# Kernel tuning notes

Hardware: AMD Instinct MI355X
Metric: run time of the kernel (lower is better)

## Reference

```python
import jax, jax.numpy as jnp
import numpy as np
from jax import lax

B, L, DIN, DOUT, K = 8, 4096, 256, 256, 3


def _gates(x, W, b, k):
    # x: [B, L, Din] -> conv over time, channels-first like torch Conv1d
    xt = jnp.transpose(x, (0, 2, 1))  # [B, Din, L]
    pad = (k - 1) // 2
    g = lax.conv_general_dilated(xt, W, window_strides=(1,), padding=[(pad, pad)],
                                 dimension_numbers=("NCH", "OIH", "NCH"))
    g = g + b[None, :, None]
    g = jnp.transpose(g, (0, 2, 1))  # [B, L, 3*Dout]
    f, o, z = jnp.split(g, 3, axis=-1)
    return jax.nn.sigmoid(f), jax.nn.sigmoid(o), jnp.tanh(z)


def _fo_pool(f, z, init_cell, reverse):
    # c_t = f_t * c_{t-1} + (1 - f_t) * z_t ; scan over time axis
    fT = jnp.transpose(f, (1, 0, 2))  # [L, B, D]
    zT = jnp.transpose(z, (1, 0, 2))

    def step(c, fz):
        ft, zt = fz
        c = ft * c + (1.0 - ft) * zt
        return c, c

    _, cells = lax.scan(step, init_cell, (fT, zT), reverse=reverse)
    return jnp.transpose(cells, (1, 0, 2))  # [B, L, D]


def setup_inputs() -> dict:
    key = jax.random.key(0)
    k1, k2, k3, k4, k5, k6 = jax.random.split(key, 6)
    scale_in = 1.0 / np.sqrt(DIN * K)
    inp = {
        "input": jax.random.normal(k1, (B, L, DIN), dtype=jnp.float32),
        "lengths": jnp.full((B,), L, dtype=jnp.int64) if False else jax.random.randint(k2, (B,), 1, L + 1),
        "W_fwd": jax.random.uniform(k3, (3 * DOUT, DIN, K), dtype=jnp.float32, minval=-scale_in, maxval=scale_in),
        "b_fwd": jax.random.uniform(k4, (3 * DOUT,), dtype=jnp.float32, minval=-scale_in, maxval=scale_in),
        "W_bwd": jax.random.uniform(k5, (3 * DOUT, DIN, K), dtype=jnp.float32, minval=-scale_in, maxval=scale_in),
        "b_bwd": jax.random.uniform(k6, (3 * DOUT,), dtype=jnp.float32, minval=-scale_in, maxval=scale_in),
    }
    return inp


def reference(input, lengths, W_fwd, b_fwd, W_bwd, b_bwd):
    init_cell = jnp.zeros((input.shape[0], DOUT), dtype=input.dtype)

    # forward direction
    f, o, z = _gates(input, W_fwd, b_fwd, K)
    cell = _fo_pool(f, z, init_cell, reverse=False)
    hidden = cell * o

    # backward direction
    fr, orr, zr = _gates(input, W_bwd, b_bwd, K)
    rcell = _fo_pool(fr, zr, init_cell, reverse=True)
    rhidden = rcell * orr

    output = jnp.concatenate([hidden, rhidden], axis=-1)  # [B, L, 2*Dout]
    last_h = jnp.concatenate([hidden[:, -1, :], rhidden[:, -1, :]], axis=-1)
    last_c = jnp.concatenate([cell[:, -1, :], rcell[:, -1, :]], axis=-1)
    return output, last_h, last_c
```

## Files before the change

kernel.cpp:

```cpp
#include <hip/hip_runtime.h>
#include <hip/hip_bf16.h>
#include <hip/hip_fp16.h>

#define B_     8
#define L_     4096
#define DIN    256
#define DOUT   256
#define NGATE  1536
#define KDIM   768
#define LP     (L_ + 2)
#define CHUNK  32
#define NCHUNK (L_ / CHUNK)

typedef short    short8  __attribute__((ext_vector_type(8)));
typedef __bf16   bf16x8  __attribute__((ext_vector_type(8)));
typedef float    floatx4 __attribute__((ext_vector_type(4)));
typedef _Float16 half4   __attribute__((ext_vector_type(4)));

__device__ __forceinline__ float fast_sigmoid(float x) {
    return __builtin_amdgcn_rcpf(1.f + __expf(-x));
}
__device__ __forceinline__ float fast_tanh(float x) {
    return 1.f - 2.f * __builtin_amdgcn_rcpf(1.f + __expf(2.f * x));
}
__device__ __forceinline__ unsigned short f2bf(float x) {
    unsigned u = __float_as_uint(x);
    u += 0x7FFF + ((u >> 16) & 1);
    return (unsigned short)(u >> 16);
}
__device__ __forceinline__ void gload16(const unsigned short* g, unsigned short* l) {
    __builtin_amdgcn_global_load_lds((const __attribute__((address_space(1))) void*)g,
                                     (__attribute__((address_space(3))) void*)l,
                                     16, 0, 0);
}

__global__ void prep_x(const float* __restrict__ x, unsigned short* __restrict__ Xp) {
    int idx = blockIdx.x * 256 + threadIdx.x;
    int row = idx >> 6;
    if (row >= B_ * LP) return;
    int c4 = (idx & 63) << 2;
    int b = row / LP, r = row - b * LP;
    float4 v = make_float4(0.f, 0.f, 0.f, 0.f);
    if (r >= 1 && r <= L_) {
        v = *(const float4*)(x + ((size_t)(b * L_ + (r - 1))) * DIN + c4);
    }
    ushort4 o = make_ushort4(f2bf(v.x), f2bf(v.y), f2bf(v.z), f2bf(v.w));
    *(ushort4*)(Xp + (size_t)row * DIN + c4) = o;
}

__global__ void prep_w(const float* __restrict__ Wf, const float* __restrict__ bf_,
                       const float* __restrict__ Wb, const float* __restrict__ bb,
                       unsigned short* __restrict__ Wc, float* __restrict__ bc) {
    int gid = blockIdx.x * 256 + threadIdx.x;
    if (gid < NGATE) {
        bc[gid] = (gid < 768) ? bf_[gid] : bb[gid - 768];
    }
    if (gid >= NGATE * KDIM) return;
    int n = gid / KDIM, k = gid - n * KDIM;
    int s = k >> 8, ic = k & 255;
    const float* W = (n < 768) ? Wf : Wb;
    int oc = (n < 768) ? n : n - 768;
    float v = W[(size_t)oc * KDIM + ic * 3 + s];
    Wc[(size_t)n * KDIM + k] = f2bf(v);
}

__launch_bounds__(512)
__global__ void gemm_gates(const unsigned short* __restrict__ Xp,
                           const unsigned short* __restrict__ Wc,
                           const float* __restrict__ bc,
                           _Float16* __restrict__ gates) {
    __shared__ unsigned short As[256 * 64];
    __shared__ unsigned short Bs[128 * 64];
    const int tid  = threadIdx.x;
    const int lane = tid & 63, wave = tid >> 6;
    const int quad = lane >> 4, l16 = lane & 15;
    const int wr = wave >> 1, wcl = wave & 1;

    int flat = blockIdx.x;
    int xcd  = flat & 7;
    int slot = flat >> 3;
    int m    = xcd * 16 + slot / 12;
    int nblk = slot % 12;
    const int b  = m >> 4;
    const int t0 = (m & 15) << 8;
    const int n0 = nblk << 7;
    const unsigned short* Ab = Xp + (size_t)b * LP * DIN;

    int rowA[4], cgA[4], rowB[2], cgB[2];
#pragma unroll
    for (int j = 0; j < 4; j++) {
        int G = (wave * 4 + j) * 64 + lane;
        rowA[j] = G >> 3;
        cgA[j]  = ((G & 7) ^ (rowA[j] & 7)) * 8;
    }
#pragma unroll
    for (int j = 0; j < 2; j++) {
        int G = (wave * 2 + j) * 64 + lane;
        rowB[j] = G >> 3;
        cgB[j]  = ((G & 7) ^ (rowB[j] & 7)) * 8;
    }

    floatx4 acc[4][4];
#pragma unroll
    for (int i = 0; i < 4; i++)
#pragma unroll
        for (int j = 0; j < 4; j++) acc[i][j] = (floatx4)0.f;

    for (int k0 = 0; k0 < KDIM; k0 += 64) {
        const int sh = k0 >> 8;
        const int c0 = k0 & 255;
#pragma unroll
        for (int j = 0; j < 4; j++)
            gload16(Ab + (size_t)(t0 + rowA[j] + sh) * DIN + c0 + cgA[j],
                    &As[(wave * 4 + j) * 512]);
#pragma unroll
        for (int j = 0; j < 2; j++)
            gload16(Wc + (size_t)(n0 + rowB[j]) * KDIM + k0 + cgB[j],
                    &Bs[(wave * 2 + j) * 512]);
        __syncthreads();
#pragma unroll
        for (int kk = 0; kk < 2; kk++) {
            const int g0 = kk * 4 + quad;
            short8 af[4], bfr[4];
#pragma unroll
            for (int mi = 0; mi < 4; mi++) {
                int row = wr * 64 + mi * 16 + l16;
                af[mi] = *(const short8*)&As[row * 64 + ((g0 ^ (row & 7)) << 3)];
            }
#pragma unroll
            for (int ni = 0; ni < 4; ni++) {
                int row = wcl * 64 + ni * 16 + l16;
                bfr[ni] = *(const short8*)&Bs[row * 64 + ((g0 ^ (row & 7)) << 3)];
            }
#pragma unroll
            for (int mi = 0; mi < 4; mi++)
#pragma unroll
                for (int ni = 0; ni < 4; ni++)
                    acc[mi][ni] = __builtin_amdgcn_mfma_f32_16x16x32_bf16(
                        __builtin_bit_cast(bf16x8, af[mi]),
                        __builtin_bit_cast(bf16x8, bfr[ni]),
                        acc[mi][ni], 0, 0, 0);
        }
        __syncthreads();
    }

#pragma unroll
    for (int ni = 0; ni < 4; ni++) {
        int col = wcl * 64 + ni * 16 + l16;
        int n = n0 + col;
        float bias = bc[n];
        int cls = (n >> 8) % 3;
#pragma unroll
        for (int mi = 0; mi < 4; mi++) {
#pragma unroll
            for (int rr = 0; rr < 4; rr++) {
                int row = wr * 64 + mi * 16 + quad * 4 + rr;
                float v = acc[mi][ni][rr] + bias;
                v = (cls == 2) ? fast_tanh(v) : fast_sigmoid(v);
                gates[((size_t)(b * L_ + t0 + row)) * NGATE + n] = (_Float16)v;
            }
        }
    }
}

__global__ void scan_chunks(const _Float16* __restrict__ gates,
                            float2* __restrict__ PW) {
    const int tid = threadIdx.x;
    const int cg = tid & 63, sub = tid >> 6;
    const int s = blockIdx.x * 4 + sub, b = blockIdx.y, dir = blockIdx.z;
    const _Float16* gb = gates + (size_t)(b * L_) * NGATE + dir * 768 + cg * 4;
    float P[4] = {1.f, 1.f, 1.f, 1.f}, W[4] = {0.f, 0.f, 0.f, 0.f};
    if (dir == 0) {
        int t = s * CHUNK;
#pragma unroll 8
        for (int i = 0; i < CHUNK; i++, t++) {
            half4 f4 = *(const half4*)(gb + (size_t)t * NGATE);
            half4 z4 = *(const half4*)(gb + (size_t)t * NGATE + 512);
#pragma unroll
            for (int u = 0; u < 4; u++) {
                float f = (float)f4[u], z = (float)z4[u];
                W[u] = f * W[u] + (1.f - f) * z;
                P[u] *= f;
            }
        }
    } else {
        int t = s * CHUNK + CHUNK - 1;
#pragma unroll 8
        for (int i = 0; i < CHUNK; i++, t--) {
            half4 f4 = *(const half4*)(gb + (size_t)t * NGATE);
            half4 z4 = *(const half4*)(gb + (size_t)t * NGATE + 512);
#pragma unroll
            for (int u = 0; u < 4; u++) {
                float f = (float)f4[u], z = (float)z4[u];
                W[u] = f * W[u] + (1.f - f) * z;
                P[u] *= f;
            }
        }
    }
    float2* p = &PW[(((size_t)(dir * 8 + b)) * NCHUNK + s) * 256 + cg * 4];
    float4 o0 = make_float4(P[0], W[0], P[1], W[1]);
    float4 o1 = make_float4(P[2], W[2], P[3], W[3]);
    *(float4*)&p[0] = o0;
    *(float4*)&p[2] = o1;
}

__global__ void scan_seq(const float2* __restrict__ PW, float* __restrict__ C0) {
    const int c = threadIdx.x;
    const int dir = blockIdx.x >> 3, b = blockIdx.x & 7;
    const size_t base = ((size_t)(dir * 8 + b)) * NCHUNK * 256 + c;
    float cc = 0.f;
    if (dir == 0) {
#pragma unroll 16
        for (int s = 0; s < NCHUNK; s++) {
            float2 pw = PW[base + (size_t)s * 256];
            C0[base + (size_t)s * 256] = cc;
            cc = pw.x * cc + pw.y;
        }
    } else {
#pragma unroll 16
        for (int s = NCHUNK - 1; s >= 0; s--) {
            float2 pw = PW[base + (size_t)s * 256];
            C0[base + (size_t)s * 256] = cc;
            cc = pw.x * cc + pw.y;
        }
    }
}

__global__ void scan_final(const _Float16* __restrict__ gates,
                           const float* __restrict__ C0,
                           float* __restrict__ out) {
    const int tid = threadIdx.x;
    const int cg = tid & 63, sub = tid >> 6;
    const int s = blockIdx.x * 4 + sub, b = blockIdx.y, dir = blockIdx.z;
    const _Float16* gb = gates + (size_t)(b * L_) * NGATE + dir * 768 + cg * 4;
    float4 c = *(const float4*)&C0[(((size_t)(dir * 8 + b)) * NCHUNK + s) * 256 + cg * 4];
    float* ob = out + (size_t)(b * L_) * (2 * DOUT) + dir * DOUT + cg * 4;
    float* lasth = out + (size_t)B_ * L_ * (2 * DOUT);
    float* lastc = lasth + B_ * (2 * DOUT);
    const int step = (dir == 0) ? 1 : -1;
    int t = (dir == 0) ? s * CHUNK : s * CHUNK + CHUNK - 1;
#pragma unroll 8
    for (int i = 0; i < CHUNK; i++, t += step) {
        half4 f4 = *(const half4*)(gb + (size_t)t * NGATE);
        half4 o4 = *(const half4*)(gb + (size_t)t * NGATE + 256);
        half4 z4 = *(const half4*)(gb + (size_t)t * NGATE + 512);
        float4 h;
        {
            float f = (float)f4[0], z = (float)z4[0];
            c.x = f * c.x + (1.f - f) * z; h.x = c.x * (float)o4[0];
            f = (float)f4[1]; z = (float)z4[1];
            c.y = f * c.y + (1.f - f) * z; h.y = c.y * (float)o4[1];
            f = (float)f4[2]; z = (float)z4[2];
            c.z = f * c.z + (1.f - f) * z; h.z = c.z * (float)o4[2];
            f = (float)f4[3]; z = (float)z4[3];
            c.w = f * c.w + (1.f - f) * z; h.w = c.w * (float)o4[3];
        }
        *(float4*)&ob[(size_t)t * (2 * DOUT)] = h;
        if (t == L_ - 1) {
            *(float4*)&lasth[b * 2 * DOUT + dir * DOUT + cg * 4] = h;
            *(float4*)&lastc[b * 2 * DOUT + dir * DOUT + cg * 4] = c;
        }
    }
}

extern "C" void kernel_launch(void* const* d_in, const int* in_sizes, int n_in,
                              void* d_out, int out_size, void* d_ws, size_t ws_size,
                              hipStream_t stream) {
    const float* x   = (const float*)d_in[0];
    const float* Wf  = (const float*)d_in[2];
    const float* bfv = (const float*)d_in[3];
    const float* Wb  = (const float*)d_in[4];
    const float* bbv = (const float*)d_in[5];

    char* ws = (char*)d_ws;
    unsigned short* Xp    = (unsigned short*)(ws);
    unsigned short* Wc    = (unsigned short*)(ws + 16785408);
    float*          bc    = (float*)(ws + 19144704);
    _Float16*       gates = (_Float16*)(ws + 19150848);
    float2*         PW    = (float2*)(ws);
    float*          C0    = (float*)(ws + 4194304);
    float*          out   = (float*)d_out;

    prep_x<<<(B_ * LP * 64 + 255) / 256, 256, 0, stream>>>(x, Xp);
    prep_w<<<(NGATE * KDIM + 255) / 256, 256, 0, stream>>>(Wf, bfv, Wb, bbv, Wc, bc);
    gemm_gates<<<1536, 512, 0, stream>>>(Xp, Wc, bc, gates);
    scan_chunks<<<dim3(NCHUNK / 4, B_, 2), 256, 0, stream>>>(gates, PW);
    scan_seq<<<16, 256, 0, stream>>>(PW, C0);
    scan_final<<<dim3(NCHUNK / 4, B_, 2), 256, 0, stream>>>(gates, C0, out);
}
```

Before: 232.5 us.

## Store gates in MFMA-fragment tiled layout and remap scan threads per channel

The GEMM epilogue now writes each 4-row MFMA fragment as a contiguous half4 into a tiled gate buffer, replacing scattered 2-byte stores. The scan kernels are rewritten to one thread per channel, reading 4 consecutive timesteps per half4 load through index helpers that decode the tiled layout. The final scan transposes hidden outputs through shared memory so the output stays coalesced. The two prep kernels are also merged into one launch. In exchange, scan_final adds block barriers on every group of timesteps and the scans run as many more, smaller blocks.

New measurement: 215.8 us. 7.2% less time.

```diff
diff --git a/kernel.cpp b/kernel.cpp
--- a/kernel.cpp
+++ b/kernel.cpp
@@ -34,34 +34,45 @@
                                      16, 0, 0);
 }
 
-__global__ void prep_x(const float* __restrict__ x, unsigned short* __restrict__ Xp) {
-    int idx = blockIdx.x * 256 + threadIdx.x;
-    int row = idx >> 6;
-    if (row >= B_ * LP) return;
-    int c4 = (idx & 63) << 2;
-    int b = row / LP, r = row - b * LP;
-    float4 v = make_float4(0.f, 0.f, 0.f, 0.f);
-    if (r >= 1 && r <= L_) {
-        v = *(const float4*)(x + ((size_t)(b * L_ + (r - 1))) * DIN + c4);
-    }
-    ushort4 o = make_ushort4(f2bf(v.x), f2bf(v.y), f2bf(v.z), f2bf(v.w));
-    *(ushort4*)(Xp + (size_t)row * DIN + c4) = o;
-}
-
-__global__ void prep_w(const float* __restrict__ Wf, const float* __restrict__ bf_,
-                       const float* __restrict__ Wb, const float* __restrict__ bb,
-                       unsigned short* __restrict__ Wc, float* __restrict__ bc) {
-    int gid = blockIdx.x * 256 + threadIdx.x;
-    if (gid < NGATE) {
-        bc[gid] = (gid < 768) ? bf_[gid] : bb[gid - 768];
-    }
-    if (gid >= NGATE * KDIM) return;
-    int n = gid / KDIM, k = gid - n * KDIM;
-    int s = k >> 8, ic = k & 255;
-    const float* W = (n < 768) ? Wf : Wb;
-    int oc = (n < 768) ? n : n - 768;
-    float v = W[(size_t)oc * KDIM + ic * 3 + s];
-    Wc[(size_t)n * KDIM + k] = f2bf(v);
+__device__ __forceinline__ int gate_noff(int n) {
+    return (n >> 7) * 32768 + ((n >> 6) & 1) * 4096 + ((n >> 4) & 3) * 1024 + (n & 15) * 4;
+}
+__device__ __forceinline__ int gate_toff(int b, int t) {
+    return (b * 16 + (t >> 8)) * 393216 + ((t >> 6) & 3) * 8192
+         + ((t >> 4) & 3) * 256 + ((t >> 2) & 3) * 64;
+}
+
+#define NXB ((B_ * LP * 64 + 255) / 256)
+#define NWB ((NGATE * KDIM + 255) / 256)
+__global__ void prep_all(const float* __restrict__ x, unsigned short* __restrict__ Xp,
+                         const float* __restrict__ Wf, const float* __restrict__ bf_,
+                         const float* __restrict__ Wb, const float* __restrict__ bb,
+                         unsigned short* __restrict__ Wc, float* __restrict__ bc) {
+    if (blockIdx.x < NXB) {
+        int idx = blockIdx.x * 256 + threadIdx.x;
+        int row = idx >> 6;
+        if (row >= B_ * LP) return;
+        int c4 = (idx & 63) << 2;
+        int b = row / LP, r = row - b * LP;
+        float4 v = make_float4(0.f, 0.f, 0.f, 0.f);
+        if (r >= 1 && r <= L_) {
+            v = *(const float4*)(x + ((size_t)(b * L_ + (r - 1))) * DIN + c4);
+        }
+        ushort4 o = make_ushort4(f2bf(v.x), f2bf(v.y), f2bf(v.z), f2bf(v.w));
+        *(ushort4*)(Xp + (size_t)row * DIN + c4) = o;
+    } else {
+        int gid = (blockIdx.x - NXB) * 256 + threadIdx.x;
+        if (gid < NGATE) {
+            bc[gid] = (gid < 768) ? bf_[gid] : bb[gid - 768];
+        }
+        if (gid >= NGATE * KDIM) return;
+        int n = gid / KDIM, k = gid - n * KDIM;
+        int s = k >> 8, ic = k & 255;
+        const float* W = (n < 768) ? Wf : Wb;
+        int oc = (n < 768) ? n : n - 768;
+        float v = W[(size_t)oc * KDIM + ic * 3 + s];
+        Wc[(size_t)n * KDIM + k] = f2bf(v);
+    }
 }
 
 __launch_bounds__(512)
@@ -79,10 +90,10 @@
     int flat = blockIdx.x;
     int xcd  = flat & 7;
     int slot = flat >> 3;
-    int m    = xcd * 16 + slot / 12;
+    int bm   = xcd * 16 + slot / 12;
     int nblk = slot % 12;
-    const int b  = m >> 4;
-    const int t0 = (m & 15) << 8;
+    const int b  = bm >> 4;
+    const int t0 = (bm & 15) << 8;
     const int n0 = nblk << 7;
     const unsigned short* Ab = Xp + (size_t)b * LP * DIN;
 
@@ -144,64 +155,62 @@
         __syncthreads();
     }
 
+    const int cls = ((n0 + wcl * 64) >> 8) % 3;
+    _Float16* gb = gates + ((size_t)(bm * 12 + nblk) * 8 + wave) * 4096 + lane * 4;
 #pragma unroll
     for (int ni = 0; ni < 4; ni++) {
-        int col = wcl * 64 + ni * 16 + l16;
-        int n = n0 + col;
-        float bias = bc[n];
-        int cls = (n >> 8) % 3;
+        float bias = bc[n0 + wcl * 64 + ni * 16 + l16];
 #pragma unroll
         for (int mi = 0; mi < 4; mi++) {
+            half4 hv;
 #pragma unroll
             for (int rr = 0; rr < 4; rr++) {
-                int row = wr * 64 + mi * 16 + quad * 4 + rr;
                 float v = acc[mi][ni][rr] + bias;
                 v = (cls == 2) ? fast_tanh(v) : fast_sigmoid(v);
-                gates[((size_t)(b * L_ + t0 + row)) * NGATE + n] = (_Float16)v;
-            }
+                hv[rr] = (_Float16)v;
+            }
+            *(half4*)(gb + (ni * 4 + mi) * 256) = hv;
         }
     }
 }
 
 __global__ void scan_chunks(const _Float16* __restrict__ gates,
                             float2* __restrict__ PW) {
-    const int tid = threadIdx.x;
-    const int cg = tid & 63, sub = tid >> 6;
-    const int s = blockIdx.x * 4 + sub, b = blockIdx.y, dir = blockIdx.z;
-    const _Float16* gb = gates + (size_t)(b * L_) * NGATE + dir * 768 + cg * 4;
-    float P[4] = {1.f, 1.f, 1.f, 1.f}, W[4] = {0.f, 0.f, 0.f, 0.f};
+    const int d = threadIdx.x;
+    const int s = blockIdx.x, b = blockIdx.y, dir = blockIdx.z;
+    const int onf = gate_noff(dir * 768 + d);
+    const int onz = gate_noff(dir * 768 + 512 + d);
+    float P = 1.f, W = 0.f;
     if (dir == 0) {
-        int t = s * CHUNK;
-#pragma unroll 8
-        for (int i = 0; i < CHUNK; i++, t++) {
-            half4 f4 = *(const half4*)(gb + (size_t)t * NGATE);
-            half4 z4 = *(const half4*)(gb + (size_t)t * NGATE + 512);
+#pragma unroll
+        for (int gi = 0; gi < 8; gi++) {
+            int t = s * CHUNK + gi * 4;
+            int ot = gate_toff(b, t);
+            half4 f4 = *(const half4*)(gates + ot + onf);
+            half4 z4 = *(const half4*)(gates + ot + onz);
 #pragma unroll
             for (int u = 0; u < 4; u++) {
                 float f = (float)f4[u], z = (float)z4[u];
-                W[u] = f * W[u] + (1.f - f) * z;
-                P[u] *= f;
+                W = f * W + (1.f - f) * z;
+                P *= f;
             }
         }
     } else {
-        int t = s * CHUNK + CHUNK - 1;
-#pragma unroll 8
-        for (int i = 0; i < CHUNK; i++, t--) {
-            half4 f4 = *(const half4*)(gb + (size_t)t * NGATE);
-            half4 z4 = *(const half4*)(gb + (size_t)t * NGATE + 512);
-#pragma unroll
-            for (int u = 0; u < 4; u++) {
+#pragma unroll
+        for (int gi = 7; gi >= 0; gi--) {
+            int t = s * CHUNK + gi * 4;
+            int ot = gate_toff(b, t);
+            half4 f4 = *(const half4*)(gates + ot + onf);
+            half4 z4 = *(const half4*)(gates + ot + onz);
+#pragma unroll
+            for (int u = 3; u >= 0; u--) {
                 float f = (float)f4[u], z = (float)z4[u];
-                W[u] = f * W[u] + (1.f - f) * z;
-                P[u] *= f;
-            }
-        }
-    }
-    float2* p = &PW[(((size_t)(dir * 8 + b)) * NCHUNK + s) * 256 + cg * 4];
-    float4 o0 = make_float4(P[0], W[0], P[1], W[1]);
-    float4 o1 = make_float4(P[2], W[2], P[3], W[3]);
-    *(float4*)&p[0] = o0;
-    *(float4*)&p[2] = o1;
+                W = f * W + (1.f - f) * z;
+                P *= f;
+            }
+        }
+    }
+    PW[(((size_t)(dir * 8 + b)) * NCHUNK + s) * 256 + d] = make_float2(P, W);
 }
 
 __global__ void scan_seq(const float2* __restrict__ PW, float* __restrict__ C0) {
@@ -229,37 +238,56 @@
 __global__ void scan_final(const _Float16* __restrict__ gates,
                            const float* __restrict__ C0,
                            float* __restrict__ out) {
-    const int tid = threadIdx.x;
-    const int cg = tid & 63, sub = tid >> 6;
-    const int s = blockIdx.x * 4 + sub, b = blockIdx.y, dir = blockIdx.z;
-    const _Float16* gb = gates + (size_t)(b * L_) * NGATE + dir * 768 + cg * 4;
-    float4 c = *(const float4*)&C0[(((size_t)(dir * 8 + b)) * NCHUNK + s) * 256 + cg * 4];
-    float* ob = out + (size_t)(b * L_) * (2 * DOUT) + dir * DOUT + cg * 4;
+    __shared__ float hbuf[4][256];
+    const int d = threadIdx.x;
+    const int s = blockIdx.x, b = blockIdx.y, dir = blockIdx.z;
+    const int onf = gate_noff(dir * 768 + d);
+    const int ono = gate_noff(dir * 768 + 256 + d);
+    const int onz = gate_noff(dir * 768 + 512 + d);
+    float c = C0[(((size_t)(dir * 8 + b)) * NCHUNK + s) * 256 + d];
+    float* ob = out + (size_t)(b * L_) * (2 * DOUT) + dir * DOUT;
     float* lasth = out + (size_t)B_ * L_ * (2 * DOUT);
     float* lastc = lasth + B_ * (2 * DOUT);
-    const int step = (dir == 0) ? 1 : -1;
-    int t = (dir == 0) ? s * CHUNK : s * CHUNK + CHUNK - 1;
-#pragma unroll 8
-    for (int i = 0; i < CHUNK; i++, t += step) {
-        half4 f4 = *(const half4*)(gb + (size_t)t * NGATE);
-        half4 o4 = *(const half4*)(gb + (size_t)t * NGATE + 256);
-        half4 z4 = *(const half4*)(gb + (size_t)t * NGATE + 512);
-        float4 h;
-        {
-            float f = (float)f4[0], z = (float)z4[0];
-            c.x = f * c.x + (1.f - f) * z; h.x = c.x * (float)o4[0];
-            f = (float)f4[1]; z = (float)z4[1];
-            c.y = f * c.y + (1.f - f) * z; h.y = c.y * (float)o4[1];
-            f = (float)f4[2]; z = (float)z4[2];
-            c.z = f * c.z + (1.f - f) * z; h.z = c.z * (float)o4[2];
-            f = (float)f4[3]; z = (float)z4[3];
-            c.w = f * c.w + (1.f - f) * z; h.w = c.w * (float)o4[3];
-        }
-        *(float4*)&ob[(size_t)t * (2 * DOUT)] = h;
-        if (t == L_ - 1) {
-            *(float4*)&lasth[b * 2 * DOUT + dir * DOUT + cg * 4] = h;
-            *(float4*)&lastc[b * 2 * DOUT + dir * DOUT + cg * 4] = c;
-        }
+    const int tl = d >> 6, cl = (d & 63) * 4;
+
+    for (int gg = 0; gg < 8; gg++) {
+        int gi = (dir == 0) ? gg : 7 - gg;
+        int t = s * CHUNK + gi * 4;
+        int ot = gate_toff(b, t);
+        half4 f4 = *(const half4*)(gates + ot + onf);
+        half4 o4 = *(const half4*)(gates + ot + ono);
+        half4 z4 = *(const half4*)(gates + ot + onz);
+        float h[4];
+        if (dir == 0) {
+#pragma unroll
+            for (int u = 0; u < 4; u++) {
+                float f = (float)f4[u], z = (float)z4[u];
+                c = f * c + (1.f - f) * z;
+                h[u] = c * (float)o4[u];
+            }
+            if (s == NCHUNK - 1 && gi == 7) {
+                lasth[b * 2 * DOUT + d] = h[3];
+                lastc[b * 2 * DOUT + d] = c;
+            }
+        } else {
+#pragma unroll
+            for (int u = 3; u >= 0; u--) {
+                float f = (float)f4[u], z = (float)z4[u];
+                c = f * c + (1.f - f) * z;
+                h[u] = c * (float)o4[u];
+                if (u == 3 && s == NCHUNK - 1 && gi == 7) {
+                    lasth[b * 2 * DOUT + DOUT + d] = h[3];
+                    lastc[b * 2 * DOUT + DOUT + d] = c;
+                }
+            }
+        }
+        hbuf[0][d] = h[0];
+        hbuf[1][d] = h[1];
+        hbuf[2][d] = h[2];
+        hbuf[3][d] = h[3];
+        __syncthreads();
+        *(float4*)&ob[(size_t)(t + tl) * (2 * DOUT) + cl] = *(float4*)&hbuf[tl][cl];
+        __syncthreads();
     }
 }
 
@@ -281,10 +309,9 @@
     float*          C0    = (float*)(ws + 4194304);
     float*          out   = (float*)d_out;
 
-    prep_x<<<(B_ * LP * 64 + 255) / 256, 256, 0, stream>>>(x, Xp);
-    prep_w<<<(NGATE * KDIM + 255) / 256, 256, 0, stream>>>(Wf, bfv, Wb, bbv, Wc, bc);
+    prep_all<<<NXB + NWB, 256, 0, stream>>>(x, Xp, Wf, bfv, Wb, bbv, Wc, bc);
     gemm_gates<<<1536, 512, 0, stream>>>(Xp, Wc, bc, gates);
-    scan_chunks<<<dim3(NCHUNK / 4, B_, 2), 256, 0, stream>>>(gates, PW);
+    scan_chunks<<<dim3(NCHUNK, B_, 2), 256, 0, stream>>>(gates, PW);
     scan_seq<<<16, 256, 0, stream>>>(PW, C0);
-    scan_final<<<dim3(NCHUNK / 4, B_, 2), 256, 0, stream>>>(gates, C0, out);
-}
+    scan_final<<<dim3(NCHUNK, B_, 2), 256, 0, stream>>>(gates, C0, out);
+}
```
